# Performance work log

Measured on AMD Instinct MI355X. Metric: run time of the kernel, lower is better.

Reference implementation:

```python
import jax, jax.numpy as jnp
import numpy as np

NEG_INF = -9e15  # mask value used by the original dense GAT
ALPHA = 0.2      # LeakyReLU negative slope


def _gat_layer(x, adj_mask, W, a1, a2, concat):
    # x: [N, F], W: [F, D], a1/a2: [D]
    Wh = x @ W                                   # [N, D]
    # e_ij = leakyrelu(a1.Wh_i + a2.Wh_j)
    e = jax.nn.leaky_relu((Wh @ a1)[:, None] + (Wh @ a2)[None, :], negative_slope=ALPHA)
    e = jnp.where(adj_mask, e, NEG_INF)          # [N, N]
    att = jax.nn.softmax(e, axis=1)              # masked row softmax
    h = att @ Wh                                 # [N, D]
    return jax.nn.elu(h) if concat else h


def setup_inputs() -> dict:
    key = jax.random.key(0)
    ks = jax.random.split(key, 8)
    N, F, D, H, O = 4096, 512, 64, 8, 128
    x = jax.random.normal(ks[0], (N, F), dtype=jnp.float32)
    adj = jax.random.randint(ks[1], (N, N), 0, 2, dtype=jnp.int32)
    # per-head params (stacked for vmap)
    W_heads = jax.random.normal(ks[2], (H, F, D), dtype=jnp.float32) * 0.05
    a1_heads = jax.random.normal(ks[3], (H, D), dtype=jnp.float32) * 0.05
    a2_heads = jax.random.normal(ks[4], (H, D), dtype=jnp.float32) * 0.05
    # output attention layer: in = H*D, out = O
    W_out = jax.random.normal(ks[5], (H * D, O), dtype=jnp.float32) * 0.05
    a1_out = jax.random.normal(ks[6], (O,), dtype=jnp.float32) * 0.05
    a2_out = jax.random.normal(ks[7], (O,), dtype=jnp.float32) * 0.05
    return {"x": x, "adj": adj, "W_heads": W_heads, "a1_heads": a1_heads,
            "a2_heads": a2_heads, "W_out": W_out, "a1_out": a1_out, "a2_out": a2_out}


def reference(x, adj, W_heads, a1_heads, a2_heads, W_out, a1_out, a2_out):
    adj_mask = adj > 0                           # [N, N] bool
    # multi-head attention (concat=True -> ELU), vmapped over heads
    heads = jax.vmap(lambda W, a1, a2: _gat_layer(x, adj_mask, W, a1, a2, True))(
        W_heads, a1_heads, a2_heads)             # [H, N, D]
    H, N, D = heads.shape
    h = jnp.transpose(heads, (1, 0, 2)).reshape(N, H * D)  # concat dim=1
    # dropout is identity at inference
    out = _gat_layer(h, adj_mask, W_out, a1_out, a2_out, False)  # [N, O]
    return out
```

## Files before the change

kernel.cpp:

```cpp
#include <hip/hip_runtime.h>
#include <hip/hip_bf16.h>
#include <cstdint>


using bf16_t = __bf16;
using half_t = _Float16;
using bf16x4 = __attribute__((ext_vector_type(4))) __bf16;
using bf16x8 = __attribute__((ext_vector_type(8))) __bf16;
using f16x4  = __attribute__((ext_vector_type(4))) _Float16;
using f16x8  = __attribute__((ext_vector_type(8))) _Float16;
using f32x4  = __attribute__((ext_vector_type(4))) float;

#define LOG2E 1.44269504f
constexpr int NN = 4096;

__global__ __launch_bounds__(256) void pack_bits_k(const int* __restrict__ adj,
                                                   uint32_t* __restrict__ bitsT, int total) {
    int stride = gridDim.x * blockDim.x;
    for (int idx = blockIdx.x * blockDim.x + threadIdx.x; idx < total; idx += stride) {
        unsigned long long m = __ballot(adj[idx] > 0);
        int l = threadIdx.x & 63;
        int i = idx >> 12, j = idx & 4095;
        if (l == 0)        bitsT[(size_t)(j >> 5) * NN + i] = (uint32_t)m;
        else if (l == 32)  bitsT[(size_t)(j >> 5) * NN + i] = (uint32_t)(m >> 32);
    }
}

__global__ __launch_bounds__(256) void prep_k(const float* __restrict__ x,
                                              const float* __restrict__ Wh,
                                              const float* __restrict__ Wo,
                                              bf16_t* __restrict__ xbt,
                                              bf16_t* __restrict__ WT1t,
                                              bf16_t* __restrict__ WoutT) {
    const int NXT = NN * 512 / 8;
    const int NWT = 512 * 512 / 8;
    const int NW2 = 128 * 512;
    int stride = gridDim.x * blockDim.x;
    for (int t = blockIdx.x * blockDim.x + threadIdx.x; t < NXT + NWT + NW2; t += stride) {
        if (t < NXT) {
            size_t d = (size_t)t * 8;
            int kc = (int)(d >> 17);
            int rem = (int)(d & 131071);
            int i = rem >> 5, k0 = rem & 31;
            const float* sp = x + (size_t)i * 512 + kc * 32 + k0;
            f32x4 s0 = *(const f32x4*)sp;
            f32x4 s1 = *(const f32x4*)(sp + 4);
            bf16x8 o;
#pragma unroll
            for (int e = 0; e < 4; ++e) { o[e] = (bf16_t)s0[e]; o[4 + e] = (bf16_t)s1[e]; }
            *(bf16x8*)(xbt + d) = o;
        } else if (t < NXT + NWT) {
            size_t d = (size_t)(t - NXT) * 8;
            int kc = (int)(d >> 14);
            int rem = (int)(d & 16383);
            int col = rem >> 5, k0 = rem & 31;
            int h = col >> 6, dd = col & 63;
            bf16x8 o;
#pragma unroll
            for (int e = 0; e < 8; ++e)
                o[e] = (bf16_t)Wh[(size_t)(h << 15) + (size_t)(kc * 32 + k0 + e) * 64 + dd];
            *(bf16x8*)(WT1t + d) = o;
        } else {
            int u = t - NXT - NWT;
            int o2 = u >> 9, cc = u & 511;
            WoutT[u] = (bf16_t)Wo[cc * 128 + o2];
        }
    }
}

template<int CS, int WC, int TILED>
__global__ __launch_bounds__(256) void gemm_k(const bf16_t* __restrict__ A,
                                              const bf16_t* __restrict__ BT,
                                              half_t* __restrict__ VTt,
                                              float* __restrict__ Cp,
                                              const float* __restrict__ a1,
                                              const float* __restrict__ a2,
                                              float* __restrict__ g1,
                                              float* __restrict__ E2,
                                              float* __restrict__ F2,
                                              int K, int NC, int kslice, int NCOLS) {
    const int wave = threadIdx.x >> 6, lane = threadIdx.x & 63;
    const int lr = lane & 15, kg = lane >> 4;
    const int rowb = (blockIdx.x * 4 + wave) * 16, cb = blockIdx.y * 64, kz = blockIdx.z;
    f32x4 acc[4];
#pragma unroll
    for (int dt = 0; dt < 4; ++dt) acc[dt] = 0.0f;
    const int k0beg = kz * kslice, k0end = k0beg + kslice;
    for (int k0 = k0beg; k0 < k0end; k0 += 32) {
        bf16x8 af;
        if (TILED) {
            const int kc = k0 >> 5;
            af = *(const bf16x8*)(A + (size_t)kc * (NN * 32) + (size_t)(rowb + lr) * 32 + kg * 8);
        } else {
            af = *(const bf16x8*)(A + (size_t)(rowb + lr) * K + k0 + kg * 8);
        }
#pragma unroll
        for (int dt = 0; dt < 4; ++dt) {
            bf16x8 bfr;
            if (TILED) {
                const int kc = k0 >> 5;
                bfr = *(const bf16x8*)(BT + (size_t)kc * (NC * 32) +
                                       (size_t)(cb + dt * 16 + lr) * 32 + kg * 8);
            } else {
                bfr = *(const bf16x8*)(BT + (size_t)(cb + dt * 16 + lr) * K + k0 + kg * 8);
            }
            acc[dt] = __builtin_amdgcn_mfma_f32_16x16x32_bf16(af, bfr, acc[dt], 0, 0, 0);
        }
    }
    if (WC) {
#pragma unroll
        for (int dt = 0; dt < 4; ++dt)
#pragma unroll
            for (int r = 0; r < 4; ++r)
                Cp[((size_t)kz * NN + rowb + kg * 4 + r) * NC + cb + dt * 16 + lr] = acc[dt][r];
    }
    if (CS) {
        const int i0 = rowb + kg * 4;
        const size_t tbase = (size_t)(i0 >> 5) * NCOLS * 32 + (i0 & 31);
#pragma unroll
        for (int dt = 0; dt < 4; ++dt) {
            f16x4 v;
#pragma unroll
            for (int r = 0; r < 4; ++r) v[r] = (half_t)acc[dt][r];
            *(f16x4*)(VTt + tbase + (size_t)(cb + dt * 16 + lr) * 32) = v;
        }
        float a1v[4], a2v[4];
#pragma unroll
        for (int dt = 0; dt < 4; ++dt) {
            a1v[dt] = a1[cb + dt * 16 + lr];
            a2v[dt] = a2[cb + dt * 16 + lr];
        }
#pragma unroll
        for (int r = 0; r < 4; ++r) {
            float d1 = 0.f, d2 = 0.f;
#pragma unroll
            for (int dt = 0; dt < 4; ++dt) { d1 += acc[dt][r] * a1v[dt]; d2 += acc[dt][r] * a2v[dt]; }
#pragma unroll
            for (int o = 1; o < 16; o <<= 1) { d1 += __shfl_xor(d1, o); d2 += __shfl_xor(d2, o); }
            if (lr == 0) {
                size_t row = (size_t)blockIdx.y * NN + rowb + kg * 4 + r;
                g1[row] = exp2f(-0.8f * LOG2E * d1);
                E2[row] = exp2f(LOG2E * d2);
                F2[row] = exp2f(0.2f * LOG2E * d2);
            }
        }
    }
}

template<int NW, int JZG>
__global__ __launch_bounds__(64 * NW) void gat_agg_k(const float* __restrict__ g1,
                                                     const float* __restrict__ E2,
                                                     const float* __restrict__ F2, int shead,
                                                     const uint32_t* __restrict__ bitsT,
                                                     const half_t* __restrict__ VTt,
                                                     bf16_t* __restrict__ Hpart,
                                                     float* __restrict__ zpart,
                                                     int CT, int JR, int ZC, int TS) {
    const int wave = threadIdx.x >> 6, lane = threadIdx.x & 63;
    const int lr = lane & 15, kg = lane >> 4;
    const int c = blockIdx.x / JZG, jzg = blockIdx.x % JZG;
    const int rowb = blockIdx.y * 64;
    const int jz = jzg * NW + wave;
    const int cb = c * 64;
    const float* gp  = g1 + (size_t)shead * c;
    const float* E2p = E2 + (size_t)shead * c;
    const float* F2p = F2 + (size_t)shead * c;
    const int steps = JR >> 5, jb0 = jz * JR;

    f32x4 acc[4][4], accz[4];
#pragma unroll
    for (int rt = 0; rt < 4; ++rt) {
        accz[rt] = 0.0f;
#pragma unroll
        for (int dt = 0; dt < 4; ++dt) acc[rt][dt] = 0.0f;
    }
    float gv[4];
#pragma unroll
    for (int rt = 0; rt < 4; ++rt) gv[rt] = gp[rowb + rt * 16 + lr];
    f16x8 ones;
#pragma unroll
    for (int e = 0; e < 8; ++e) ones[e] = (half_t)(lr == 0 ? 1.0f : 0.0f);

    auto LOAD = [&](int jb, f16x8* bfr, f32x4& e2a, f32x4& e2b, f32x4& f2a, f32x4& f2b,
                    uint32_t* bw) {
        const int jk = jb + kg * 8;
        const int jc = jb >> 5;
        e2a = *(const f32x4*)(E2p + jk);
        e2b = *(const f32x4*)(E2p + jk + 4);
        f2a = *(const f32x4*)(F2p + jk);
        f2b = *(const f32x4*)(F2p + jk + 4);
        const half_t* vb = VTt + (size_t)jc * TS + kg * 8;
#pragma unroll
        for (int dt = 0; dt < 4; ++dt)
            bfr[dt] = *(const f16x8*)(vb + (size_t)(cb + dt * 16 + lr) * 32);
        const uint32_t* bb = bitsT + (size_t)jc * NN + rowb;
#pragma unroll
        for (int rt = 0; rt < 4; ++rt)
            bw[rt] = bb[rt * 16 + lr];
    };
    auto COMP = [&](const f16x8* bfr, f32x4 e2a, f32x4 e2b, f32x4 f2a, f32x4 f2b,
                    const uint32_t* bw) {
#pragma unroll
        for (int rt = 0; rt < 4; ++rt) {
            uint32_t mb = (bw[rt] >> (kg * 8)) & 0xffu;
            f16x8 af;
#pragma unroll
            for (int e = 0; e < 8; ++e) {
                float e2 = (e < 4) ? e2a[e] : e2b[e - 4];
                float f2 = (e < 4) ? f2a[e] : f2b[e - 4];
                float p = fmaxf(e2, gv[rt] * f2);
                p = (mb & (1u << e)) ? p : 0.0f;
                af[e] = (half_t)p;
            }
#pragma unroll
            for (int dt = 0; dt < 4; ++dt)
                acc[rt][dt] = __builtin_amdgcn_mfma_f32_16x16x32_f16(af, bfr[dt], acc[rt][dt], 0, 0, 0);
            accz[rt] = __builtin_amdgcn_mfma_f32_16x16x32_f16(af, ones, accz[rt], 0, 0, 0);
        }
    };

    f16x8 bA[4], bB[4];
    f32x4 eaA, ebA, faA, fbA, eaB, ebB, faB, fbB;
    uint32_t wA[4], wB[4];
    LOAD(jb0, bA, eaA, ebA, faA, fbA, wA);
    for (int js = 0; js < steps - 2; js += 2) {
        LOAD(jb0 + (js + 1) * 32, bB, eaB, ebB, faB, fbB, wB);
        COMP(bA, eaA, ebA, faA, fbA, wA);
        LOAD(jb0 + (js + 2) * 32, bA, eaA, ebA, faA, fbA, wA);
        COMP(bB, eaB, ebB, faB, fbB, wB);
    }
    LOAD(jb0 + (steps - 1) * 32, bB, eaB, ebB, faB, fbB, wB);
    COMP(bA, eaA, ebA, faA, fbA, wA);
    COMP(bB, eaB, ebB, faB, fbB, wB);

    bf16_t* Hp = Hpart + (size_t)jz * NN * CT;
#pragma unroll
    for (int rt = 0; rt < 4; ++rt) {
#pragma unroll
        for (int dt = 0; dt < 4; ++dt)
#pragma unroll
            for (int r = 0; r < 4; ++r)
                Hp[(size_t)(rowb + rt * 16 + kg * 4 + r) * CT + cb + dt * 16 + lr] = (bf16_t)acc[rt][dt][r];
    }
    if (lr == 0 && (ZC > 1 || c == 0)) {
        int zi = jz * ZC + (ZC > 1 ? c : 0);
#pragma unroll
        for (int rt = 0; rt < 4; ++rt)
#pragma unroll
            for (int r = 0; r < 4; ++r)
                zpart[(size_t)zi * NN + rowb + rt * 16 + kg * 4 + r] = accz[rt][r];
    }
}

__global__ __launch_bounds__(256) void fin1_k(const bf16_t* __restrict__ Hpart,
                                              const float* __restrict__ zpart,
                                              bf16_t* __restrict__ hcatb) {
    int idx = blockIdx.x * 256 + threadIdx.x;
    int i = idx >> 6, col0 = (idx & 63) << 3, h = col0 >> 6;
    float Z = 0.f;
#pragma unroll
    for (int jz = 0; jz < 8; ++jz) Z += zpart[(size_t)(jz * 8 + h) * NN + i];
    float hs[8];
#pragma unroll
    for (int e = 0; e < 8; ++e) hs[e] = 0.f;
#pragma unroll
    for (int jz = 0; jz < 8; ++jz) {
        bf16x8 v = *(const bf16x8*)(Hpart + ((size_t)jz * NN + i) * 512 + col0);
#pragma unroll
        for (int e = 0; e < 8; ++e) hs[e] += (float)v[e];
    }
    float invZ = 1.0f / Z;
    bf16x8 o;
#pragma unroll
    for (int e = 0; e < 8; ++e) {
        float v = hs[e] * invZ;
        o[e] = (bf16_t)(v > 0.f ? v : expm1f(v));
    }
    *(bf16x8*)(hcatb + (size_t)i * 512 + col0) = o;
}

__global__ __launch_bounds__(128) void comb2_k(const float* __restrict__ Cp,
                                               const float* __restrict__ a1o,
                                               const float* __restrict__ a2o,
                                               half_t* __restrict__ VT2t,
                                               float* __restrict__ g1o,
                                               float* __restrict__ E2o,
                                               float* __restrict__ F2o) {
    int r = blockIdx.x, t = threadIdx.x;
    float w = 0.f;
#pragma unroll
    for (int z = 0; z < 4; ++z) w += Cp[((size_t)z * NN + r) * 128 + t];
    VT2t[(size_t)(r >> 5) * (128 * 32) + t * 32 + (r & 31)] = (half_t)w;
    float d1 = w * a1o[t], d2 = w * a2o[t];
#pragma unroll
    for (int o = 1; o < 64; o <<= 1) { d1 += __shfl_xor(d1, o); d2 += __shfl_xor(d2, o); }
    __shared__ float red[4];
    if ((t & 63) == 0) { red[(t >> 6) * 2 + 0] = d1; red[(t >> 6) * 2 + 1] = d2; }
    __syncthreads();
    if (t == 0) {
        float s1 = red[0] + red[2], s2 = red[1] + red[3];
        g1o[r] = exp2f(-0.8f * LOG2E * s1);
        E2o[r] = exp2f(LOG2E * s2);
        F2o[r] = exp2f(0.2f * LOG2E * s2);
    }
}

__global__ __launch_bounds__(256) void fin2_k(const bf16_t* __restrict__ Hpart,
                                              const float* __restrict__ zpart,
                                              float* __restrict__ out) {
    int idx = blockIdx.x * 256 + threadIdx.x;
    int i = idx >> 4, col0 = (idx & 15) << 3;
    float Z = 0.f;
#pragma unroll
    for (int jz = 0; jz < 16; ++jz) Z += zpart[(size_t)jz * NN + i];
    float hs[8];
#pragma unroll
    for (int e = 0; e < 8; ++e) hs[e] = 0.f;
#pragma unroll
    for (int jz = 0; jz < 16; ++jz) {
        bf16x8 v = *(const bf16x8*)(Hpart + ((size_t)jz * NN + i) * 128 + col0);
#pragma unroll
        for (int e = 0; e < 8; ++e) hs[e] += (float)v[e];
    }
    float invZ = 1.0f / Z;
    f32x4 o0, o1;
#pragma unroll
    for (int e = 0; e < 4; ++e) { o0[e] = hs[e] * invZ; o1[e] = hs[e + 4] * invZ; }
    *(f32x4*)(out + (size_t)i * 128 + col0) = o0;
    *(f32x4*)(out + (size_t)i * 128 + col0 + 4) = o1;
}

extern "C" void kernel_launch(void* const* d_in, const int* in_sizes, int n_in,
                              void* d_out, int out_size, void* d_ws, size_t ws_size,
                              hipStream_t stream) {
    const int N = 4096;
    const float* x       = (const float*)d_in[0];
    const int*   adj     = (const int*)d_in[1];
    const float* W_heads = (const float*)d_in[2];
    const float* a1h     = (const float*)d_in[3];
    const float* a2h     = (const float*)d_in[4];
    const float* W_out   = (const float*)d_in[5];
    const float* a1o     = (const float*)d_in[6];
    const float* a2o     = (const float*)d_in[7];
    (void)in_sizes; (void)n_in; (void)out_size; (void)ws_size;

    size_t off = 0;
    auto alloc = [&](size_t bytes) { size_t o = off; off = (off + bytes + 255) & ~(size_t)255; return o; };
    char* ws = (char*)d_ws;
    uint32_t* bitsT = (uint32_t*)(ws + alloc((size_t)N * N / 8));
    half_t* VT1t    = (half_t*)(ws + alloc((size_t)512 * N * 2));
    bf16_t* hcatb   = (bf16_t*)(ws + alloc((size_t)N * 512 * 2));
    bf16_t* WoutT   = (bf16_t*)(ws + alloc((size_t)128 * 512 * 2));
    float*  g1h     = (float*)(ws + alloc((size_t)8 * N * 4));
    float*  E2h     = (float*)(ws + alloc((size_t)8 * N * 4));
    float*  F2h     = (float*)(ws + alloc((size_t)8 * N * 4));
    float*  g1o     = (float*)(ws + alloc((size_t)N * 4));
    float*  E2o     = (float*)(ws + alloc((size_t)N * 4));
    float*  F2o     = (float*)(ws + alloc((size_t)N * 4));
    half_t* VT2t    = (half_t*)(ws + alloc((size_t)128 * N * 2));
    float*  zpart   = (float*)(ws + alloc((size_t)64 * N * 4));
    bf16_t* Hpart   = (bf16_t*)(ws + alloc((size_t)32 * 1024 * 1024));
    bf16_t* xbt   = (bf16_t*)Hpart;
    bf16_t* WT1t  = (bf16_t*)((char*)Hpart + (9 << 20));
    float*  Cpart = (float*)Hpart;

    hipLaunchKernelGGL(pack_bits_k, dim3(2048), dim3(256), 0, stream, adj, bitsT, N * N);
    hipLaunchKernelGGL(prep_k, dim3(1024), dim3(256), 0, stream, x, W_heads, W_out, xbt, WT1t, WoutT);
    hipLaunchKernelGGL((gemm_k<1, 0, 1>), dim3(64, 8, 1), dim3(256), 0, stream,
                       xbt, WT1t, VT1t, (float*)nullptr, a1h, a2h, g1h, E2h, F2h, 512, 512, 512, 512);
    hipLaunchKernelGGL((gat_agg_k<8, 1>), dim3(8, 64, 1), dim3(512), 0, stream,
                       g1h, E2h, F2h, N, bitsT, VT1t, Hpart, zpart, 512, 512, 8, 512 * 32);
    hipLaunchKernelGGL(fin1_k, dim3(1024), dim3(256), 0, stream, Hpart, zpart, hcatb);
    hipLaunchKernelGGL((gemm_k<0, 1, 0>), dim3(64, 2, 4), dim3(256), 0, stream,
                       hcatb, WoutT, (half_t*)nullptr, Cpart,
                       (const float*)nullptr, (const float*)nullptr,
                       (float*)nullptr, (float*)nullptr, (float*)nullptr, 512, 128, 128, 128);
    hipLaunchKernelGGL(comb2_k, dim3(4096), dim3(128), 0, stream, Cpart, a1o, a2o, VT2t, g1o, E2o, F2o);
    hipLaunchKernelGGL((gat_agg_k<4, 4>), dim3(8, 64, 1), dim3(256), 0, stream,
                       g1o, E2o, F2o, 0, bitsT, VT2t, Hpart, zpart, 128, 256, 1, 128 * 32);
    hipLaunchKernelGGL(fin2_k, dim3(256), dim3(256), 0, stream, Hpart, zpart, (float*)d_out);
}
```

Measured before the change: 138.4 us.

## Fuse adjacency bit-packing into prep kernel and halve first aggregation's K-split

Folds the adjacency-to-bitmask packing into the prep kernel. Each thread now reads 32 contiguous ints with vector loads and writes one transposed bit word directly, replacing the ballot-based kernel and removing one launch. Separately, the first-layer aggregation moves from 8 waves and an 8-way split over neighbors to 4 waves and a 1024-column slice, and fin1 now reduces only 4 partials instead of 8. This means fewer partial buffers to write and read back, in exchange for more sequential work per block and fewer concurrent waves.

Measured after the change: 133.3 us. 3.7% less time.

```diff
diff --git a/kernel.cpp b/kernel.cpp
--- a/kernel.cpp
+++ b/kernel.cpp
@@ -14,31 +14,35 @@
 #define LOG2E 1.44269504f
 constexpr int NN = 4096;
 
-__global__ __launch_bounds__(256) void pack_bits_k(const int* __restrict__ adj,
-                                                   uint32_t* __restrict__ bitsT, int total) {
-    int stride = gridDim.x * blockDim.x;
-    for (int idx = blockIdx.x * blockDim.x + threadIdx.x; idx < total; idx += stride) {
-        unsigned long long m = __ballot(adj[idx] > 0);
-        int l = threadIdx.x & 63;
-        int i = idx >> 12, j = idx & 4095;
-        if (l == 0)        bitsT[(size_t)(j >> 5) * NN + i] = (uint32_t)m;
-        else if (l == 32)  bitsT[(size_t)(j >> 5) * NN + i] = (uint32_t)(m >> 32);
-    }
-}
-
-__global__ __launch_bounds__(256) void prep_k(const float* __restrict__ x,
+__global__ __launch_bounds__(256) void prep_k(const int* __restrict__ adj,
+                                              const float* __restrict__ x,
                                               const float* __restrict__ Wh,
                                               const float* __restrict__ Wo,
+                                              uint32_t* __restrict__ bitsT,
                                               bf16_t* __restrict__ xbt,
                                               bf16_t* __restrict__ WT1t,
                                               bf16_t* __restrict__ WoutT) {
+    const int NB  = NN * NN / 32;
     const int NXT = NN * 512 / 8;
     const int NWT = 512 * 512 / 8;
     const int NW2 = 128 * 512;
     int stride = gridDim.x * blockDim.x;
-    for (int t = blockIdx.x * blockDim.x + threadIdx.x; t < NXT + NWT + NW2; t += stride) {
-        if (t < NXT) {
-            size_t d = (size_t)t * 8;
+    for (int t = blockIdx.x * blockDim.x + threadIdx.x; t < NB + NXT + NWT + NW2; t += stride) {
+        if (t < NB) {
+            int jc = t >> 12, i = t & 4095;
+            const int4* ap = (const int4*)(adj + (size_t)i * NN + jc * 32);
+            uint32_t w = 0;
+#pragma unroll
+            for (int q = 0; q < 8; ++q) {
+                int4 a = ap[q];
+                w |= (a.x > 0 ? 1u : 0u) << (q * 4 + 0);
+                w |= (a.y > 0 ? 1u : 0u) << (q * 4 + 1);
+                w |= (a.z > 0 ? 1u : 0u) << (q * 4 + 2);
+                w |= (a.w > 0 ? 1u : 0u) << (q * 4 + 3);
+            }
+            bitsT[t] = w;
+        } else if (t < NB + NXT) {
+            size_t d = (size_t)(t - NB) * 8;
             int kc = (int)(d >> 17);
             int rem = (int)(d & 131071);
             int i = rem >> 5, k0 = rem & 31;
@@ -49,8 +53,8 @@
 #pragma unroll
             for (int e = 0; e < 4; ++e) { o[e] = (bf16_t)s0[e]; o[4 + e] = (bf16_t)s1[e]; }
             *(bf16x8*)(xbt + d) = o;
-        } else if (t < NXT + NWT) {
-            size_t d = (size_t)(t - NXT) * 8;
+        } else if (t < NB + NXT + NWT) {
+            size_t d = (size_t)(t - NB - NXT) * 8;
             int kc = (int)(d >> 14);
             int rem = (int)(d & 16383);
             int col = rem >> 5, k0 = rem & 31;
@@ -61,7 +65,7 @@
                 o[e] = (bf16_t)Wh[(size_t)(h << 15) + (size_t)(kc * 32 + k0 + e) * 64 + dd];
             *(bf16x8*)(WT1t + d) = o;
         } else {
-            int u = t - NXT - NWT;
+            int u = t - NB - NXT - NWT;
             int o2 = u >> 9, cc = u & 511;
             WoutT[u] = (bf16_t)Wo[cc * 128 + o2];
         }
@@ -259,12 +263,12 @@
     int i = idx >> 6, col0 = (idx & 63) << 3, h = col0 >> 6;
     float Z = 0.f;
 #pragma unroll
-    for (int jz = 0; jz < 8; ++jz) Z += zpart[(size_t)(jz * 8 + h) * NN + i];
+    for (int jz = 0; jz < 4; ++jz) Z += zpart[(size_t)(jz * 8 + h) * NN + i];
     float hs[8];
 #pragma unroll
     for (int e = 0; e < 8; ++e) hs[e] = 0.f;
 #pragma unroll
-    for (int jz = 0; jz < 8; ++jz) {
+    for (int jz = 0; jz < 4; ++jz) {
         bf16x8 v = *(const bf16x8*)(Hpart + ((size_t)jz * NN + i) * 512 + col0);
 #pragma unroll
         for (int e = 0; e < 8; ++e) hs[e] += (float)v[e];
@@ -364,12 +368,12 @@
     bf16_t* WT1t  = (bf16_t*)((char*)Hpart + (9 << 20));
     float*  Cpart = (float*)Hpart;
 
-    hipLaunchKernelGGL(pack_bits_k, dim3(2048), dim3(256), 0, stream, adj, bitsT, N * N);
-    hipLaunchKernelGGL(prep_k, dim3(1024), dim3(256), 0, stream, x, W_heads, W_out, xbt, WT1t, WoutT);
+    hipLaunchKernelGGL(prep_k, dim3(2048), dim3(256), 0, stream,
+                       adj, x, W_heads, W_out, bitsT, xbt, WT1t, WoutT);
     hipLaunchKernelGGL((gemm_k<1, 0, 1>), dim3(64, 8, 1), dim3(256), 0, stream,
                        xbt, WT1t, VT1t, (float*)nullptr, a1h, a2h, g1h, E2h, F2h, 512, 512, 512, 512);
-    hipLaunchKernelGGL((gat_agg_k<8, 1>), dim3(8, 64, 1), dim3(512), 0, stream,
-                       g1h, E2h, F2h, N, bitsT, VT1t, Hpart, zpart, 512, 512, 8, 512 * 32);
+    hipLaunchKernelGGL((gat_agg_k<4, 1>), dim3(8, 64, 1), dim3(256), 0, stream,
+                       g1h, E2h, F2h, N, bitsT, VT1t, Hpart, zpart, 512, 1024, 8, 512 * 32);
     hipLaunchKernelGGL(fin1_k, dim3(1024), dim3(256), 0, stream, Hpart, zpart, hcatb);
     hipLaunchKernelGGL((gemm_k<0, 1, 0>), dim3(64, 2, 4), dim3(256), 0, stream,
                        hcatb, WoutT, (half_t*)nullptr, Cpart,
```
